# Optimization experiments

Hardware: AMD Instinct MI355X
Metric: run time of the kernel (lower is better)

Reference implementation:

```python
import jax, jax.numpy as jnp
import numpy as np

N_NODES = 100000
N_EDGES = 1600000
HIDDEN = 128
NUM_FEAT = 1
NUM_CLASSES = 10
NUM_GRAPHS = 512


def setup_inputs() -> dict:
    key = jax.random.key(0)
    ks = jax.random.split(key, 16)
    x = jax.random.normal(ks[0], (N_NODES, NUM_FEAT), dtype=jnp.float32)
    edge_index = jax.random.randint(ks[1], (2, N_EDGES), 0, N_NODES, dtype=jnp.int64)
    batch = jnp.sort(jax.random.randint(ks[2], (N_NODES,), 0, NUM_GRAPHS, dtype=jnp.int64))
    def glorot(k, shape):
        lim = float(np.sqrt(6.0 / (shape[0] + shape[1])))
        return jax.random.uniform(k, shape, jnp.float32, -lim, lim)
    params = {
        'W1': glorot(ks[3], (NUM_FEAT, HIDDEN)), 'b1': jnp.zeros((HIDDEN,), jnp.float32),
        'W2': glorot(ks[4], (HIDDEN, HIDDEN)), 'b2': jnp.zeros((HIDDEN,), jnp.float32),
        'W3': glorot(ks[5], (HIDDEN, HIDDEN)), 'b3': jnp.zeros((HIDDEN,), jnp.float32),
        'W4': glorot(ks[6], (HIDDEN, HIDDEN)), 'b4': jnp.zeros((HIDDEN,), jnp.float32),
        'W5': glorot(ks[7], (HIDDEN, HIDDEN)), 'b5': jnp.zeros((HIDDEN,), jnp.float32),
        'Wlin': glorot(ks[8], (HIDDEN, NUM_CLASSES)), 'blin': jnp.zeros((NUM_CLASSES,), jnp.float32),
    }
    return {'x': x, 'edge_index': edge_index, 'batch': batch, **params}


def _gcn_norm(edge_index, n_nodes):
    # PyG GCNConv: add self-loops, sym-normalize by deg^-1/2 on both ends.
    loops = jnp.arange(n_nodes, dtype=edge_index.dtype)
    src = jnp.concatenate([edge_index[0], loops])
    dst = jnp.concatenate([edge_index[1], loops])
    deg = jax.ops.segment_sum(jnp.ones_like(dst, jnp.float32), dst, num_segments=n_nodes)
    dis = jnp.where(deg > 0, jax.lax.rsqrt(jnp.maximum(deg, 1.0)), 0.0)
    norm = dis[src] * dis[dst]  # [E + N]
    return src, dst, norm


def _gcn_conv(h, W, b, src, dst, norm, n_nodes):
    h = h @ W  # transform first (PyG order)
    msg = h[src] * norm[:, None]  # gather + scale, [E+N, H]
    out = jax.ops.segment_sum(msg, dst, num_segments=n_nodes)  # scatter-add
    return out + b


def reference(x, edge_index, batch, W1, b1, W2, b2, W3, b3, W4, b4, W5, b5, Wlin, blin):
    n = x.shape[0]
    src, dst, norm = _gcn_norm(edge_index, n)
    h = _gcn_conv(x, W1, b1, src, dst, norm, n)
    h = _gcn_conv(h, W2, b2, src, dst, norm, n)
    h = _gcn_conv(h, W3, b3, src, dst, norm, n)
    h = _gcn_conv(h, W4, b4, src, dst, norm, n)
    h = _gcn_conv(h, W5, b5, src, dst, norm, n)
    # global mean pool over graphs
    sums = jax.ops.segment_sum(h, batch, num_segments=NUM_GRAPHS)
    cnts = jax.ops.segment_sum(jnp.ones((n,), jnp.float32), batch, num_segments=NUM_GRAPHS)
    pooled = sums / jnp.maximum(cnts, 1.0)[:, None]
    # dropout is identity at eval
    return pooled @ Wlin + blin
```

## Files before the change

kernel.cpp:

```cpp
#include <hip/hip_runtime.h>

#define NT 256
#define BN_SHIFT 8
#define NBUCKET_MAX 512
#define CAP 8192
#define EPB 4096

__global__ void __launch_bounds__(768)
prep_kernel(const float* __restrict__ W1, const float* __restrict__ b1,
            const float* __restrict__ W2, const float* __restrict__ b2,
            const float* __restrict__ W3, const float* __restrict__ b3,
            const float* __restrict__ W4, const float* __restrict__ b4,
            const float* __restrict__ W5, const float* __restrict__ b5,
            const float* __restrict__ Wlin, float* __restrict__ qout,
            int* __restrict__ gcur, int NB) {
  __shared__ float cur[6][128];
  const int tid = threadIdx.x;
  for (int i = tid; i < NB; i += 768) gcur[i] = 0;
  const int vi = tid >> 7;
  const int t = tid & 127;
  float init;
  if (vi == 0) init = W1[t];
  else if (vi == 1) init = b1[t];
  else if (vi == 2) init = b2[t];
  else if (vi == 3) init = b3[t];
  else if (vi == 4) init = b4[t];
  else init = b5[t];
  cur[vi][t] = init;
  __syncthreads();
  const float* Ws[4] = {W2, W3, W4, W5};
  #pragma unroll
  for (int l = 0; l < 4; ++l) {
    const int nact = l + 2;
    float s = 0.f;
    if (vi < nact) {
      const float* __restrict__ W = Ws[l];
      #pragma unroll 8
      for (int k = 0; k < 128; ++k) s += cur[vi][k] * W[k * 128 + t];
    }
    __syncthreads();
    if (vi < nact) cur[vi][t] = s;
    __syncthreads();
  }
  if (tid < 60) {
    int v = tid / 10, c = tid % 10;
    float s = 0.f;
    for (int k = 0; k < 128; ++k) s += cur[v][k] * Wlin[k * 10 + c];
    qout[v * 10 + c] = s;
  }
}

__global__ void binA_kernel(const int* __restrict__ ei, int* __restrict__ gcur,
                            unsigned int* __restrict__ dump, int E, int NB) {
  __shared__ unsigned int cnt[NBUCKET_MAX];
  __shared__ unsigned int base[NBUCKET_MAX];
  const int t = threadIdx.x;
  const int e0 = blockIdx.x * EPB;
  for (int b = t; b < NB; b += 256) cnt[b] = 0;
  __syncthreads();
  unsigned int slot[16];
  unsigned int dreg[16];
  #pragma unroll
  for (int j = 0; j < 16; ++j) {
    int e = e0 + j * 256 + t;
    if (e < E) {
      unsigned int d = (unsigned int)ei[E + e];
      dreg[j] = d;
      slot[j] = atomicAdd(&cnt[d >> BN_SHIFT], 1u);
    }
  }
  __syncthreads();
  for (int b = t; b < NB; b += 256) {
    unsigned int c = cnt[b];
    base[b] = c ? (unsigned int)atomicAdd(&gcur[b], (int)c) : 0u;
  }
  __syncthreads();
  #pragma unroll
  for (int j = 0; j < 16; ++j) {
    int e = e0 + j * 256 + t;
    if (e < E) {
      unsigned int s = (unsigned int)ei[e];
      unsigned int d = dreg[j];
      unsigned int b = d >> BN_SHIFT;
      unsigned int pos = base[b] + slot[j];
      if (pos < CAP)
        dump[(size_t)b * CAP + pos] = (s << BN_SHIFT) | (d & 255u);
    }
  }
}

__global__ void binB_kernel(const unsigned int* __restrict__ dump,
                            const int* __restrict__ gcur,
                            const float* __restrict__ x, int* __restrict__ col,
                            int2* __restrict__ rl, float* __restrict__ dis2,
                            float* __restrict__ sq, float2* __restrict__ ta, int N) {
  __shared__ int cnt[256];
  __shared__ int sc[256];
  __shared__ int cur[256];
  const int b = blockIdx.x, t = threadIdx.x;
  cnt[t] = 0;
  __syncthreads();
  int total = gcur[b];
  if (total > CAP) total = CAP;
  const unsigned int* seg = dump + (size_t)b * CAP;
  for (int i = t; i < total; i += 256) atomicAdd(&cnt[seg[i] & 255u], 1);
  __syncthreads();
  int v = cnt[t];
  sc[t] = v;
  __syncthreads();
  for (int off = 1; off < 256; off <<= 1) {
    int u = (t >= off) ? sc[t - off] : 0;
    __syncthreads();
    sc[t] += u;
    __syncthreads();
  }
  int rbase = b * CAP + sc[t] - v;
  cur[t] = rbase;
  __syncthreads();
  for (int i = t; i < total; i += 256) {
    unsigned int w = seg[i];
    int slot = atomicAdd(&cur[w & 255u], 1);
    col[slot] = (int)(w >> BN_SHIFT);
  }
  int node = (b << BN_SHIFT) + t;
  if (node < N) {
    rl[node] = make_int2(rbase, v);
    float dis = rsqrtf((float)v + 1.0f);
    dis2[node] = dis * dis;
    sq[node] = 1.0f / dis;
    ta[node] = make_float2(dis * x[node], dis);
  }
}

__global__ void gather_kernel(const int* __restrict__ col, const int2* __restrict__ rl,
                              const float* __restrict__ dis2,
                              const float2* __restrict__ tin, float2* __restrict__ tout,
                              float* __restrict__ ssave, int N) {
  int tid = blockIdx.x * blockDim.x + threadIdx.x;
  int node = tid >> 2, l4 = tid & 3;
  if (node >= N) return;
  int2 r = rl[node];
  float sx = 0.f, sy = 0.f;
  int j = l4;
  for (; j + 4 < r.y; j += 8) {
    int c0 = col[r.x + j];
    int c1 = col[r.x + j + 4];
    float2 a0 = tin[c0];
    float2 a1 = tin[c1];
    sx += a0.x + a1.x;
    sy += a0.y + a1.y;
  }
  if (j < r.y) {
    float2 a = tin[col[r.x + j]];
    sx += a.x;
    sy += a.y;
  }
  sx += __shfl_xor(sx, 1);
  sx += __shfl_xor(sx, 2);
  sy += __shfl_xor(sy, 1);
  sy += __shfl_xor(sy, 2);
  if (l4 == 0) {
    float2 ts = tin[node];
    float m = dis2[node];
    float oy = m * (sy + ts.y);
    tout[node] = make_float2(m * (sx + ts.x), oy);
    if (ssave) ssave[node] = oy;
  }
}

__device__ __forceinline__ int lower_bound_i(const int* a, int n, int key) {
  int lo = 0, hi = n;
  while (lo < hi) {
    int mid = (lo + hi) >> 1;
    if (a[mid] < key) lo = mid + 1; else hi = mid;
  }
  return lo;
}

__global__ void pool_kernel(const int* __restrict__ batch, int N,
                            const float2* __restrict__ t5, const float* __restrict__ s4,
                            const float* __restrict__ s3, const float* __restrict__ s2,
                            const float* __restrict__ s1, const float* __restrict__ sq,
                            const float* __restrict__ q, const float* __restrict__ blin,
                            float* __restrict__ out) {
  int g = blockIdx.x;
  __shared__ int sh[2];
  if (threadIdx.x == 0) {
    sh[0] = lower_bound_i(batch, N, g);
    sh[1] = lower_bound_i(batch, N, g + 1);
  }
  __syncthreads();
  int lo = sh[0], hi = sh[1];
  float a[5] = {0.f, 0.f, 0.f, 0.f, 0.f};
  for (int i = lo + threadIdx.x; i < hi; i += blockDim.x) {
    float qq = sq[i];
    a[0] += t5[i].x * qq;
    a[1] += s4[i] * qq;
    a[2] += s3[i] * qq;
    a[3] += s2[i] * qq;
    a[4] += s1[i] * qq;
  }
  __shared__ float red[4][5];
  __shared__ float m5[5];
  int lane = threadIdx.x & 63, wave = threadIdx.x >> 6;
  #pragma unroll
  for (int j = 0; j < 5; ++j)
    #pragma unroll
    for (int o = 32; o > 0; o >>= 1) a[j] += __shfl_down(a[j], o);
  if (lane == 0)
    #pragma unroll
    for (int j = 0; j < 5; ++j) red[wave][j] = a[j];
  __syncthreads();
  if (threadIdx.x == 0) {
    float denom = fmaxf((float)(hi - lo), 1.0f);
    #pragma unroll
    for (int j = 0; j < 5; ++j)
      m5[j] = (red[0][j] + red[1][j] + red[2][j] + red[3][j]) / denom;
  }
  __syncthreads();
  int t = threadIdx.x;
  if (t < 10) {
    out[g * 10 + t] = m5[0] * q[t] + m5[1] * q[10 + t] + m5[2] * q[20 + t] +
                      m5[3] * q[30 + t] + m5[4] * q[40 + t] + q[50 + t] + blin[t];
  }
}

extern "C" void kernel_launch(void* const* d_in, const int* in_sizes, int n_in,
                              void* d_out, int out_size, void* d_ws, size_t ws_size,
                              hipStream_t stream) {
  const float* x    = (const float*)d_in[0];
  const int*   ei   = (const int*)d_in[1];
  const int*   batch= (const int*)d_in[2];
  const float* W1   = (const float*)d_in[3];
  const float* b1   = (const float*)d_in[4];
  const float* W2   = (const float*)d_in[5];
  const float* b2   = (const float*)d_in[6];
  const float* W3   = (const float*)d_in[7];
  const float* b3   = (const float*)d_in[8];
  const float* W4   = (const float*)d_in[9];
  const float* b4   = (const float*)d_in[10];
  const float* W5   = (const float*)d_in[11];
  const float* b5   = (const float*)d_in[12];
  const float* Wlin = (const float*)d_in[13];
  const float* blin = (const float*)d_in[14];

  const int N  = in_sizes[0];
  const int E  = in_sizes[1] / 2;
  const int G  = out_size / 10;
  const int NB = (N + 255) >> BN_SHIFT;

  float* ws = (float*)d_ws;
  size_t off = 0;
  float2* ta   = (float2*)(ws + off); off += 2 * (size_t)N;
  float2* tb   = (float2*)(ws + off); off += 2 * (size_t)N;
  float*  dis2 = ws + off;            off += N;
  float*  sq   = ws + off;            off += N;
  float*  s1   = ws + off;            off += N;
  float*  s2   = ws + off;            off += N;
  float*  s3   = ws + off;            off += N;
  float*  s4   = ws + off;            off += N;
  float*  qv   = ws + off;            off += 64;
  if (off & 1) off++;
  int2* rl     = (int2*)(ws + off);   off += 2 * (size_t)N;
  int* gcur    = (int*)(ws + off);    off += NB;
  if (off & 1) off++;
  unsigned int* dump = (unsigned int*)(ws + off); off += (size_t)NB * CAP;
  int* col     = (int*)(ws + off);    off += (size_t)NB * CAP;
  (void)ws_size;

  const int gridA = (E + EPB - 1) / EPB;
  const int gridG = (4 * N + NT - 1) / NT;

  prep_kernel<<<1, 768, 0, stream>>>(W1, b1, W2, b2, W3, b3, W4, b4, W5, b5,
                                     Wlin, qv, gcur, NB);
  binA_kernel<<<gridA, 256, 0, stream>>>(ei, gcur, dump, E, NB);
  binB_kernel<<<NB, 256, 0, stream>>>(dump, gcur, x, col, rl, dis2, sq, ta, N);

  gather_kernel<<<gridG, NT, 0, stream>>>(col, rl, dis2, ta, tb, s1, N);
  gather_kernel<<<gridG, NT, 0, stream>>>(col, rl, dis2, tb, ta, s2, N);
  gather_kernel<<<gridG, NT, 0, stream>>>(col, rl, dis2, ta, tb, s3, N);
  gather_kernel<<<gridG, NT, 0, stream>>>(col, rl, dis2, tb, ta, s4, N);
  gather_kernel<<<gridG, NT, 0, stream>>>(col, rl, dis2, ta, tb, nullptr, N);

  pool_kernel<<<G, 256, 0, stream>>>(batch, N, tb, s4, s3, s2, s1, sq, qv, blin,
                                     (float*)d_out);
}
```

Baseline: 130.9 us.

## Vectorize edge loads in binning, cache dump words in registers, widen gather lanes

binA now reads edge indices as int4 (four per thread per step) instead of scalar strided loads. binB keeps the dump words in a 32-entry register array between the count and scatter passes, so the segment is not re-read from global memory. The gather kernel uses 8 lanes per node instead of 4, with one extra shuffle step, to give more memory parallelism per node at average degree around 16. The register array and the larger gather grid may lower occupancy, and changing the lane grouping changes the float summation order.

```diff
diff --git a/kernel.cpp b/kernel.cpp
--- a/kernel.cpp
+++ b/kernel.cpp
@@ -56,17 +56,33 @@
   __shared__ unsigned int base[NBUCKET_MAX];
   const int t = threadIdx.x;
   const int e0 = blockIdx.x * EPB;
+  const bool vec_ok = ((E & 3) == 0);
   for (int b = t; b < NB; b += 256) cnt[b] = 0;
   __syncthreads();
   unsigned int slot[16];
   unsigned int dreg[16];
   #pragma unroll
-  for (int j = 0; j < 16; ++j) {
-    int e = e0 + j * 256 + t;
-    if (e < E) {
-      unsigned int d = (unsigned int)ei[E + e];
-      dreg[j] = d;
-      slot[j] = atomicAdd(&cnt[d >> BN_SHIFT], 1u);
+  for (int jj = 0; jj < 4; ++jj) {
+    int e = e0 + jj * 1024 + t * 4;
+    if (vec_ok && e + 3 < E) {
+      int4 d4 = *reinterpret_cast<const int4*>(&ei[E + e]);
+      dreg[jj * 4 + 0] = (unsigned)d4.x;
+      dreg[jj * 4 + 1] = (unsigned)d4.y;
+      dreg[jj * 4 + 2] = (unsigned)d4.z;
+      dreg[jj * 4 + 3] = (unsigned)d4.w;
+      #pragma unroll
+      for (int k = 0; k < 4; ++k)
+        slot[jj * 4 + k] = atomicAdd(&cnt[dreg[jj * 4 + k] >> BN_SHIFT], 1u);
+    } else {
+      #pragma unroll
+      for (int k = 0; k < 4; ++k) {
+        int ee = e + k;
+        if (ee < E) {
+          unsigned d = (unsigned)ei[E + ee];
+          dreg[jj * 4 + k] = d;
+          slot[jj * 4 + k] = atomicAdd(&cnt[d >> BN_SHIFT], 1u);
+        }
+      }
     }
   }
   __syncthreads();
@@ -76,15 +92,26 @@
   }
   __syncthreads();
   #pragma unroll
-  for (int j = 0; j < 16; ++j) {
-    int e = e0 + j * 256 + t;
-    if (e < E) {
-      unsigned int s = (unsigned int)ei[e];
-      unsigned int d = dreg[j];
-      unsigned int b = d >> BN_SHIFT;
-      unsigned int pos = base[b] + slot[j];
-      if (pos < CAP)
-        dump[(size_t)b * CAP + pos] = (s << BN_SHIFT) | (d & 255u);
+  for (int jj = 0; jj < 4; ++jj) {
+    int e = e0 + jj * 1024 + t * 4;
+    unsigned s4v[4];
+    bool fast = (vec_ok && e + 3 < E);
+    if (fast) {
+      int4 s4 = *reinterpret_cast<const int4*>(&ei[e]);
+      s4v[0] = (unsigned)s4.x; s4v[1] = (unsigned)s4.y;
+      s4v[2] = (unsigned)s4.z; s4v[3] = (unsigned)s4.w;
+    }
+    #pragma unroll
+    for (int k = 0; k < 4; ++k) {
+      int ee = e + k;
+      if (ee < E) {
+        unsigned s = fast ? s4v[k] : (unsigned)ei[ee];
+        unsigned d = dreg[jj * 4 + k];
+        unsigned b = d >> BN_SHIFT;
+        unsigned pos = base[b] + slot[jj * 4 + k];
+        if (pos < CAP)
+          dump[(size_t)b * CAP + pos] = (s << BN_SHIFT) | (d & 255u);
+      }
     }
   }
 }
@@ -103,7 +130,16 @@
   int total = gcur[b];
   if (total > CAP) total = CAP;
   const unsigned int* seg = dump + (size_t)b * CAP;
-  for (int i = t; i < total; i += 256) atomicAdd(&cnt[seg[i] & 255u], 1);
+  unsigned wreg[CAP / 256];
+  #pragma unroll
+  for (int k = 0; k < CAP / 256; ++k) {
+    int i = (k << 8) + t;
+    if (i < total) {
+      unsigned w = seg[i];
+      wreg[k] = w;
+      atomicAdd(&cnt[w & 255u], 1);
+    }
+  }
   __syncthreads();
   int v = cnt[t];
   sc[t] = v;
@@ -117,10 +153,14 @@
   int rbase = b * CAP + sc[t] - v;
   cur[t] = rbase;
   __syncthreads();
-  for (int i = t; i < total; i += 256) {
-    unsigned int w = seg[i];
-    int slot = atomicAdd(&cur[w & 255u], 1);
-    col[slot] = (int)(w >> BN_SHIFT);
+  #pragma unroll
+  for (int k = 0; k < CAP / 256; ++k) {
+    int i = (k << 8) + t;
+    if (i < total) {
+      unsigned w = wreg[k];
+      int slot = atomicAdd(&cur[w & 255u], 1);
+      col[slot] = (int)(w >> BN_SHIFT);
+    }
   }
   int node = (b << BN_SHIFT) + t;
   if (node < N) {
@@ -137,14 +177,14 @@
                               const float2* __restrict__ tin, float2* __restrict__ tout,
                               float* __restrict__ ssave, int N) {
   int tid = blockIdx.x * blockDim.x + threadIdx.x;
-  int node = tid >> 2, l4 = tid & 3;
+  int node = tid >> 3, l8 = tid & 7;
   if (node >= N) return;
   int2 r = rl[node];
   float sx = 0.f, sy = 0.f;
-  int j = l4;
-  for (; j + 4 < r.y; j += 8) {
+  int j = l8;
+  for (; j + 8 < r.y; j += 16) {
     int c0 = col[r.x + j];
-    int c1 = col[r.x + j + 4];
+    int c1 = col[r.x + j + 8];
     float2 a0 = tin[c0];
     float2 a1 = tin[c1];
     sx += a0.x + a1.x;
@@ -157,9 +197,11 @@
   }
   sx += __shfl_xor(sx, 1);
   sx += __shfl_xor(sx, 2);
+  sx += __shfl_xor(sx, 4);
   sy += __shfl_xor(sy, 1);
   sy += __shfl_xor(sy, 2);
-  if (l4 == 0) {
+  sy += __shfl_xor(sy, 4);
+  if (l8 == 0) {
     float2 ts = tin[node];
     float m = dis2[node];
     float oy = m * (sy + ts.y);
@@ -269,7 +311,7 @@
   (void)ws_size;
 
   const int gridA = (E + EPB - 1) / EPB;
-  const int gridG = (4 * N + NT - 1) / NT;
+  const int gridG = (8 * N + NT - 1) / NT;
 
   prep_kernel<<<1, 768, 0, stream>>>(W1, b1, W2, b2, W3, b3, W4, b4, W5, b5,
                                      Wlin, qv, gcur, NB);
```

Result: faster. 126.1 us (-3.6%).
